# Kernel tuning notes

Measured on AMD Instinct MI355X. Metric: run time of the kernel, lower is better.

The kernel has to match this reference:

```python
import jax, jax.numpy as jnp
import numpy as np

N = 65536      # nodes (256x256 grid)
E = 1048576    # edges (avg degree 16)
T_IN = 10      # TIME_STEPS_IN
L = 64         # LATENT_DIMS
MID = 128      # LATENT_DIMS * MLP_RATIO
GD = 2         # grid dims


def _lin_init(key, fan_in, fan_out):
    kw, kb = jax.random.split(key)
    s = 1.0 / np.sqrt(fan_in)
    W = jax.random.uniform(kw, (fan_in, fan_out), jnp.float32, -s, s)
    b = jax.random.uniform(kb, (fan_out,), jnp.float32, -s, s)
    return W, b


def setup_inputs() -> dict:
    key = jax.random.key(0)
    ks = jax.random.split(key, 10)
    x = jax.random.normal(ks[0], (N, T_IN), jnp.float32)
    grid = jax.random.uniform(ks[1], (N, GD), jnp.float32)
    edge_index = jax.random.randint(ks[2], (2, E), 0, N, jnp.int64)
    W_proj1, b_proj1 = _lin_init(ks[3], T_IN + GD, MID)
    W_proj2, b_proj2 = _lin_init(ks[4], MID, L)
    Wk, bk = _lin_init(ks[5], 2 * L + 2 * GD + 1, L)   # K edge MLP (single linear)
    Ww, bw = _lin_init(ks[6], L, L)                     # W node MLP (single linear)
    W_dec1, b_dec1 = _lin_init(ks[7], L, MID)
    W_dec2, b_dec2 = _lin_init(ks[8], MID, 1)
    return {"x": x, "grid": grid, "edge_index": edge_index,
            "W_proj1": W_proj1, "b_proj1": b_proj1, "W_proj2": W_proj2, "b_proj2": b_proj2,
            "Wk": Wk, "bk": bk, "Ww": Ww, "bw": bw,
            "W_dec1": W_dec1, "b_dec1": b_dec1, "W_dec2": W_dec2, "b_dec2": b_dec2}


def _gelu(x):
    return jax.nn.gelu(x, approximate=False)  # torch F.gelu default = exact erf


def reference(x, grid, edge_index, W_proj1, b_proj1, W_proj2, b_proj2,
              Wk, bk, Ww, bw, W_dec1, b_dec1, W_dec2, b_dec2):
    # project: cat(x, grid) -> Linear -> GELU -> Linear
    h = jnp.concatenate([x, grid], axis=-1)               # [N, T_IN+2]
    h = _gelu(h @ W_proj1 + b_proj1) @ W_proj2 + b_proj2  # [N, L]

    # message passing block (PyG source_to_target: j = row 0, i = row 1)
    src = edge_index[0]
    dst = edge_index[1]
    x_j = h[src]                                          # [E, L]
    x_i = h[dst]                                          # [E, L]
    g_j = grid[src]                                       # [E, 2]
    g_i = grid[dst]                                       # [E, 2]
    dist = jnp.sqrt(jnp.sum(jnp.square(g_i - g_j), axis=-1, keepdims=True))  # [E, 1]
    ef = jnp.concatenate([dist, g_i, g_j, x_i, x_j], axis=-1)  # [E, 2L+5]
    msg = ef @ Wk + bk                                    # [E, L]
    aggr = jax.ops.segment_sum(msg, dst, num_segments=N)  # [N, L]
    h = _gelu(h @ Ww + bw + aggr)                         # update

    # decode: Linear -> GELU -> Linear
    out = _gelu(h @ W_dec1 + b_dec1) @ W_dec2 + b_dec2    # [N, 1]
    return out
```

## Files before the change

kernel.cpp:

```cpp
#include <hip/hip_runtime.h>
#include <hip/hip_fp16.h>

static __device__ __forceinline__ float gelu(float x) {
    return 0.5f * x * (1.0f + erff(x * 0.70710678118654752f));
}

#define CAPR 32

typedef _Float16 v8h __attribute__((ext_vector_type(8)));
typedef float    v4f __attribute__((ext_vector_type(4)));
typedef int      v4i __attribute__((ext_vector_type(4)));
union F8 { uint4 u; v8h v; _Float16 f[8]; };

static __device__ __forceinline__ void acc8(float* a, uint4 u) {
    float2 f0 = __half22float2(*(__half2*)&u.x);
    float2 f1 = __half22float2(*(__half2*)&u.y);
    float2 f2 = __half22float2(*(__half2*)&u.z);
    float2 f3 = __half22float2(*(__half2*)&u.w);
    a[0] += f0.x; a[1] += f0.y; a[2] += f1.x; a[3] += f1.y;
    a[4] += f2.x; a[5] += f2.y; a[6] += f3.x; a[7] += f3.y;
}

static __device__ __forceinline__ uint4 pack8(const float* v) {
    __half2 p0 = __floats2half2_rn(v[0], v[1]);
    __half2 p1 = __floats2half2_rn(v[2], v[3]);
    __half2 p2 = __floats2half2_rn(v[4], v[5]);
    __half2 p3 = __floats2half2_rn(v[6], v[7]);
    uint4 u;
    u.x = *(unsigned*)&p0; u.y = *(unsigned*)&p1;
    u.z = *(unsigned*)&p2; u.w = *(unsigned*)&p3;
    return u;
}

__global__ void __launch_bounds__(256, 4)
k_enc_scat(const float* __restrict__ x,
           const float* __restrict__ grid,
           const float* __restrict__ W1,
           const float* __restrict__ b1,
           const float* __restrict__ W2,
           const float* __restrict__ b2,
           const int* __restrict__ ei, int* __restrict__ cnt,
           unsigned short* __restrict__ ssrc,
           __half* __restrict__ h16, int N, int E, int scatB)
{
    __shared__ uint4 tabW2[1024];
    __shared__ __half wmids[4 * 16 * 136];
    int tid = threadIdx.x;

    if ((int)blockIdx.x < scatB) {
        int p = blockIdx.x & 7;
        int c = blockIdx.x >> 3;
        const v4i* s4 = (const v4i*)ei;
        const v4i* d4 = (const v4i*)(ei + E);
        int g4 = (E / (scatB >> 3)) >> 2;
        int base4 = c * g4;
        int shift = 31 - __clz(N >> 3);
#pragma unroll 8
        for (int g = 0; g < g4 / 256; g++) {
            int idx = base4 + g * 256 + tid;
            v4i d = __builtin_nontemporal_load(&d4[idx]);
            v4i s = __builtin_nontemporal_load(&s4[idx]);
            int q;
            if ((d[0] >> shift) == p) {
                q = atomicAdd(&cnt[(d[0] << 1) + 0], 1);
                if (q < CAPR) ssrc[((size_t)d[0] << 6) + q] = (unsigned short)s[0];
            }
            if ((d[1] >> shift) == p) {
                q = atomicAdd(&cnt[(d[1] << 1) + 1], 1);
                if (q < CAPR) ssrc[((size_t)d[1] << 6) + 32 + q] = (unsigned short)s[1];
            }
            if ((d[2] >> shift) == p) {
                q = atomicAdd(&cnt[(d[2] << 1) + 0], 1);
                if (q < CAPR) ssrc[((size_t)d[2] << 6) + q] = (unsigned short)s[2];
            }
            if ((d[3] >> shift) == p) {
                q = atomicAdd(&cnt[(d[3] << 1) + 1], 1);
                if (q < CAPR) ssrc[((size_t)d[3] << 6) + 32 + q] = (unsigned short)s[3];
            }
        }
        return;
    }

    int eb = blockIdx.x - scatB;
    int lane = tid & 63, wave = tid >> 6;
    int m = lane & 15, quad = lane >> 4;

    F8 w1f[8];
#pragma unroll
    for (int nt = 0; nt < 8; nt++) {
        int col = nt * 16 + m;
        int k0 = quad << 3;
#pragma unroll
        for (int j = 0; j < 8; j++)
            w1f[nt].f[j] = (k0 + j < 12) ? (_Float16)W1[(k0 + j) * 128 + col] : (_Float16)0.f;
    }

    for (int idx = tid; idx < 1024; idx += 256) {
        int l2 = idx & 63, nt = (idx >> 6) & 3, kc = idx >> 8;
        int col = nt * 16 + (l2 & 15);
        int k0 = kc * 32 + ((l2 >> 4) << 3);
        F8 f;
#pragma unroll
        for (int j = 0; j < 8; j++) f.f[j] = (_Float16)W2[(k0 + j) * 64 + col];
        tabW2[idx] = f.u;
    }
    __syncthreads();

    __half* wm = &wmids[wave * 16 * 136];

    for (int t = 0; t < 2; t++) {
        int tile = eb * 8 + wave * 2 + t;
        int base = tile * 16;
        int n = base + m;
        F8 a1;
#pragma unroll
        for (int j = 0; j < 8; j++) a1.f[j] = (_Float16)0.f;
        if (quad == 0) {
            float2 x0 = *(const float2*)&x[(size_t)n * 10 + 0];
            float2 x1 = *(const float2*)&x[(size_t)n * 10 + 2];
            float2 x2 = *(const float2*)&x[(size_t)n * 10 + 4];
            float2 x3 = *(const float2*)&x[(size_t)n * 10 + 6];
            a1.f[0] = (_Float16)x0.x; a1.f[1] = (_Float16)x0.y;
            a1.f[2] = (_Float16)x1.x; a1.f[3] = (_Float16)x1.y;
            a1.f[4] = (_Float16)x2.x; a1.f[5] = (_Float16)x2.y;
            a1.f[6] = (_Float16)x3.x; a1.f[7] = (_Float16)x3.y;
        } else if (quad == 1) {
            float2 x4 = *(const float2*)&x[(size_t)n * 10 + 8];
            float2 g  = *(const float2*)&grid[(size_t)n * 2];
            a1.f[0] = (_Float16)x4.x; a1.f[1] = (_Float16)x4.y;
            a1.f[2] = (_Float16)g.x;  a1.f[3] = (_Float16)g.y;
        }
#pragma unroll
        for (int nt = 0; nt < 8; nt++) {
            int col = nt * 16 + m;
            float b = b1[col];
            v4f acc = {b, b, b, b};
            acc = __builtin_amdgcn_mfma_f32_16x16x32_f16(a1.v, w1f[nt].v, acc, 0, 0, 0);
#pragma unroll
            for (int reg = 0; reg < 4; reg++)
                wm[(quad * 4 + reg) * 136 + col] = __float2half(gelu(acc[reg]));
        }
        __syncthreads();

        F8 a2[4];
#pragma unroll
        for (int kc = 0; kc < 4; kc++)
            a2[kc].u = *(const uint4*)&wm[m * 136 + kc * 32 + quad * 8];
#pragma unroll
        for (int nt = 0; nt < 4; nt++) {
            int col = nt * 16 + m;
            float b = b2[col];
            v4f acc = {b, b, b, b};
#pragma unroll
            for (int kc = 0; kc < 4; kc++) {
                F8 bf; bf.u = tabW2[kc * 256 + nt * 64 + lane];
                acc = __builtin_amdgcn_mfma_f32_16x16x32_f16(a2[kc].v, bf.v, acc, 0, 0, 0);
            }
#pragma unroll
            for (int reg = 0; reg < 4; reg++)
                h16[(size_t)(base + quad * 4 + reg) * 64 + col] = __float2half(acc[reg]);
        }
        __syncthreads();
    }
}

__global__ void k_gather(const __half* __restrict__ h16,
                         const float* __restrict__ grid,
                         const unsigned short* __restrict__ ssrc,
                         const int* __restrict__ cnt,
                         __half* __restrict__ sum_h16, float* __restrict__ sum_g,
                         float* __restrict__ sum_d, int N)
{
    int tid = blockIdx.x * blockDim.x + threadIdx.x;
    int n = tid >> 3;
    int l = tid & 7;
    if (n >= N) return;
    int2 cv = *(const int2*)&cnt[n << 1];
    const uint4* h8 = (const uint4*)h16;
    float a[8] = {0,0,0,0,0,0,0,0};
    float sgx = 0.f, sgy = 0.f, sd = 0.f;
    float gix = grid[2 * n], giy = grid[2 * n + 1];
#pragma unroll
    for (int r = 0; r < 2; r++) {
        int dg = min((r == 0) ? cv.x : cv.y, CAPR);
        const unsigned short* sr = ssrc + ((size_t)n << 6) + (r << 5);
        for (int i = 0; i < dg; i += 4) {
            ushort4 sv = *(const ushort4*)&sr[i];
            int sx = sv.x, sy = sv.y, sz = sv.z, sw = sv.w;
            int rem = dg - i;
            if (rem < 4) {
                if (rem <= 1) sy = sx;
                if (rem <= 2) sz = sx;
                sw = (rem <= 3) ? sx : sw;
            }
            uint4 u0 = h8[(size_t)sx * 8 + l];
            uint4 u1 = h8[(size_t)sy * 8 + l];
            uint4 u2 = h8[(size_t)sz * 8 + l];
            uint4 u3 = h8[(size_t)sw * 8 + l];
            acc8(a, u0);
            if (rem > 1) acc8(a, u1);
            if (rem > 2) acc8(a, u2);
            if (rem > 3) acc8(a, u3);
            if (l < 4 && i + l < dg) {
                int sj = (l == 0) ? sx : (l == 1) ? sy : (l == 2) ? sz : sw;
                float2 g = *(const float2*)&grid[2 * sj];
                float dx = gix - g.x, dy = giy - g.y;
                sd += sqrtf(dx * dx + dy * dy);
                sgx += g.x; sgy += g.y;
            }
        }
    }
    sd  += __shfl_xor(sd, 1);  sd  += __shfl_xor(sd, 2);  sd  += __shfl_xor(sd, 4);
    sgx += __shfl_xor(sgx, 1); sgx += __shfl_xor(sgx, 2); sgx += __shfl_xor(sgx, 4);
    sgy += __shfl_xor(sgy, 1); sgy += __shfl_xor(sgy, 2); sgy += __shfl_xor(sgy, 4);
    ((uint4*)(sum_h16 + (size_t)n * 64))[l] = pack8(a);
    if (l == 0) { sum_d[n] = sd; sum_g[2 * n] = sgx; sum_g[2 * n + 1] = sgy; }
}

__global__ void __launch_bounds__(256, 1)
k_updec(const __half* __restrict__ h16, const __half* __restrict__ sum_h16,
        const float* __restrict__ sum_g, const float* __restrict__ sum_d,
        const int* __restrict__ cnt, const float* __restrict__ grid,
        const float* __restrict__ Wk, const float* __restrict__ bk,
        const float* __restrict__ Ww, const float* __restrict__ bw,
        const float* __restrict__ Wd1, const float* __restrict__ bd1,
        const float* __restrict__ Wd2, const float* __restrict__ bd2,
        float* __restrict__ out, int N)
{
    __shared__ uint4 tabW[512];
    __shared__ uint4 tabC[512];
    __shared__ uint4 tabD[512];
    __shared__ uint4 tabV[256];
    __shared__ uint4 tabE[1024];
    __shared__ __half h2t[4 * 16 * 72];
    int tid = threadIdx.x;

    for (int idx = tid; idx < 512; idx += 256) {
        int lane = idx & 63, nt = (idx >> 6) & 3, kc = idx >> 8;
        int col = nt * 16 + (lane & 15);
        int kr  = kc * 32 + ((lane >> 4) << 3);
        F8 fw, fc, fd;
#pragma unroll
        for (int j = 0; j < 8; j++) {
            fw.f[j] = (_Float16)Ww[(kr + j) * 64 + col];
            fc.f[j] = (_Float16)Wk[(size_t)(5 + kr + j) * 64 + col];
            fd.f[j] = (_Float16)Wk[(size_t)(69 + kr + j) * 64 + col];
        }
        tabW[idx] = fw.u; tabC[idx] = fc.u; tabD[idx] = fd.u;
    }
    if (tid < 256) {
        int lane = tid & 63, nt = tid >> 6;
        int col = nt * 16 + (lane & 15);
        F8 fv;
#pragma unroll
        for (int j = 0; j < 8; j++) fv.f[j] = (_Float16)0.f;
        if ((lane >> 4) == 0) {
            fv.f[0] = (_Float16)bw[col];
            fv.f[1] = (_Float16)bk[col];
            fv.f[2] = (_Float16)Wk[col];
            fv.f[3] = (_Float16)Wk[64 + col];
            fv.f[4] = (_Float16)Wk[128 + col];
            fv.f[5] = (_Float16)Wk[192 + col];
            fv.f[6] = (_Float16)Wk[256 + col];
        }
        tabV[tid] = fv.u;
    }
    for (int idx = tid; idx < 1024; idx += 256) {
        int lane = idx & 63, nt = (idx >> 6) & 7, kc = idx >> 9;
        int col = nt * 16 + (lane & 15);
        int kr  = kc * 32 + ((lane >> 4) << 3);
        F8 f;
#pragma unroll
        for (int j = 0; j < 8; j++) f.f[j] = (_Float16)Wd1[(kr + j) * 128 + col];
        tabE[idx] = f.u;
    }
    __syncthreads();

    int lane = tid & 63, wave = tid >> 6;
    int m = lane & 15, quad = lane >> 4;
    const uint4* h8 = (const uint4*)h16;
    const uint4* s8 = (const uint4*)sum_h16;
    __half* wt = &h2t[wave * 16 * 72];
    float bd2v = bd2[0];

    for (int t = 0; t < 2; t++) {
        int tile = blockIdx.x * 8 + wave * 2 + t;
        int base = tile * 16;
        int n = base + m;
        int2 cv = *(const int2*)&cnt[n << 1];
        float deg = (float)(min(cv.x, CAPR) + min(cv.y, CAPR));
        float sd  = sum_d[n];
        float sgx = sum_g[2 * n], sgy = sum_g[2 * n + 1];
        float gix = grid[2 * n] * deg, giy = grid[2 * n + 1] * deg;

        F8 ah0, ah1, as0, as1, ahd0, ahd1, au;
        ah0.u = h8[(size_t)n * 8 + quad];
        ah1.u = h8[(size_t)n * 8 + 4 + quad];
        as0.u = s8[(size_t)n * 8 + quad];
        as1.u = s8[(size_t)n * 8 + 4 + quad];
        _Float16 dh = (_Float16)deg;
#pragma unroll
        for (int j = 0; j < 8; j++) { ahd0.f[j] = ah0.f[j] * dh; ahd1.f[j] = ah1.f[j] * dh; }
        float z = (quad == 0) ? 1.f : 0.f;
        au.f[0] = (_Float16)z;          au.f[1] = (_Float16)(deg * z);
        au.f[2] = (_Float16)(sd * z);   au.f[3] = (_Float16)(gix * z);
        au.f[4] = (_Float16)(giy * z);  au.f[5] = (_Float16)(sgx * z);
        au.f[6] = (_Float16)(sgy * z);  au.f[7] = (_Float16)0.f;

#pragma unroll
        for (int nt = 0; nt < 4; nt++) {
            F8 bv, bw0, bw1, bc0, bc1, bd0, bd1f;
            bv.u  = tabV[nt * 64 + lane];
            bw0.u = tabW[nt * 64 + lane];       bw1.u = tabW[256 + nt * 64 + lane];
            bc0.u = tabC[nt * 64 + lane];       bc1.u = tabC[256 + nt * 64 + lane];
            bd0.u = tabD[nt * 64 + lane];       bd1f.u = tabD[256 + nt * 64 + lane];
            v4f acc = {0.f, 0.f, 0.f, 0.f};
            acc = __builtin_amdgcn_mfma_f32_16x16x32_f16(au.v,   bv.v,   acc, 0, 0, 0);
            acc = __builtin_amdgcn_mfma_f32_16x16x32_f16(ah0.v,  bw0.v,  acc, 0, 0, 0);
            acc = __builtin_amdgcn_mfma_f32_16x16x32_f16(ah1.v,  bw1.v,  acc, 0, 0, 0);
            acc = __builtin_amdgcn_mfma_f32_16x16x32_f16(ahd0.v, bc0.v,  acc, 0, 0, 0);
            acc = __builtin_amdgcn_mfma_f32_16x16x32_f16(ahd1.v, bc1.v,  acc, 0, 0, 0);
            acc = __builtin_amdgcn_mfma_f32_16x16x32_f16(as0.v,  bd0.v,  acc, 0, 0, 0);
            acc = __builtin_amdgcn_mfma_f32_16x16x32_f16(as1.v,  bd1f.v, acc, 0, 0, 0);
#pragma unroll
            for (int reg = 0; reg < 4; reg++)
                wt[(quad * 4 + reg) * 72 + m + 16 * nt] = __float2half(gelu(acc[reg]));
        }
        __syncthreads();

        F8 dh0, dh1;
        dh0.u = *(const uint4*)&wt[m * 72 + quad * 8];
        dh1.u = *(const uint4*)&wt[m * 72 + 32 + quad * 8];
        float p[4] = {0.f, 0.f, 0.f, 0.f};
#pragma unroll
        for (int nt = 0; nt < 8; nt++) {
            int col = m + 16 * nt;
            float b = bd1[col];
            float w2 = Wd2[col];
            F8 b0, b1;
            b0.u = tabE[nt * 64 + lane];
            b1.u = tabE[512 + nt * 64 + lane];
            v4f acc = {b, b, b, b};
            acc = __builtin_amdgcn_mfma_f32_16x16x32_f16(dh0.v, b0.v, acc, 0, 0, 0);
            acc = __builtin_amdgcn_mfma_f32_16x16x32_f16(dh1.v, b1.v, acc, 0, 0, 0);
#pragma unroll
            for (int reg = 0; reg < 4; reg++) p[reg] += gelu(acc[reg]) * w2;
        }
#pragma unroll
        for (int reg = 0; reg < 4; reg++) {
            p[reg] += __shfl_xor(p[reg], 1);
            p[reg] += __shfl_xor(p[reg], 2);
            p[reg] += __shfl_xor(p[reg], 4);
            p[reg] += __shfl_xor(p[reg], 8);
        }
        if (m == 0) {
#pragma unroll
            for (int reg = 0; reg < 4; reg++)
                out[base + quad * 4 + reg] = p[reg] + bd2v;
        }
        __syncthreads();
    }
}

extern "C" void kernel_launch(void* const* d_in, const int* in_sizes, int n_in,
                              void* d_out, int out_size, void* d_ws, size_t ws_size,
                              hipStream_t stream)
{
    const float* x    = (const float*)d_in[0];
    const float* grid = (const float*)d_in[1];
    const int*   ei   = (const int*)d_in[2];
    const float* W1   = (const float*)d_in[3];
    const float* b1   = (const float*)d_in[4];
    const float* W2   = (const float*)d_in[5];
    const float* b2   = (const float*)d_in[6];
    const float* Wk   = (const float*)d_in[7];
    const float* bk   = (const float*)d_in[8];
    const float* Ww   = (const float*)d_in[9];
    const float* bw   = (const float*)d_in[10];
    const float* Wd1  = (const float*)d_in[11];
    const float* bd1  = (const float*)d_in[12];
    const float* Wd2  = (const float*)d_in[13];
    const float* bd2  = (const float*)d_in[14];
    float* out = (float*)d_out;

    int N = in_sizes[0] / 10;
    int E = in_sizes[2] / 2;

    char* ws = (char*)d_ws;
    size_t o_h16  = 0;
    size_t o_sh16 = o_h16  + (size_t)N * 64 * 2;
    size_t o_sumg = o_sh16 + (size_t)N * 64 * 2;
    size_t o_sumd = o_sumg + (size_t)N * 2 * 4;
    size_t o_cnt  = o_sumd + (size_t)N * 4;
    size_t o_ssrc = o_cnt  + (size_t)N * 2 * 4;

    __half* h16     = (__half*)(ws + o_h16);
    __half* sum_h16 = (__half*)(ws + o_sh16);
    float* sum_g = (float*)(ws + o_sumg);
    float* sum_d = (float*)(ws + o_sumd);
    int*   cnt   = (int*)  (ws + o_cnt);
    unsigned short* ssrc = (unsigned short*)(ws + o_ssrc);

    hipMemsetAsync(cnt, 0, (size_t)N * 2 * 4, stream);

    int scatB = E / (256 * 4);
    int encB  = (N / 16) / 8;
    k_enc_scat<<<dim3(scatB + encB), dim3(256), 0, stream>>>(x, grid, W1, b1, W2, b2,
                                                             ei, cnt, ssrc, h16, N, E, scatB);
    k_gather<<<dim3((N * 8 + 255) / 256), dim3(256), 0, stream>>>(h16, grid, ssrc, cnt,
                                                                   sum_h16, sum_g, sum_d, N);
    int tiles = N / 16;
    k_updec<<<dim3(tiles / 8), dim3(256), 0, stream>>>(h16, sum_h16, sum_g, sum_d, cnt,
                                                       grid, Wk, bk, Ww, bw,
                                                       Wd1, bd1, Wd2, bd2, out, N);
}
```

Baseline: 206.1 us.

## Fuse neighbor gather into update/decode kernel, dropping intermediate sum buffers

Merges the gather kernel into the update/decode kernel so each wave accumulates neighbor features for its 16-node tile in registers, then feeds them straight into the MFMA update and decoder. This removes the sum_h16/sum_g/sum_d round trip through global memory and one kernel launch. The trade-off is lower gather parallelism: each lane now handles two uint4 chunks per neighbor, with 4 lanes per node instead of 8. Each block also has to rebuild the shared-memory weight tables, and twice as many blocks are launched (one tile per wave). The bias/small-weight table moves from shared memory into registers.

```diff
diff --git a/kernel.cpp b/kernel.cpp
--- a/kernel.cpp
+++ b/kernel.cpp
@@ -164,22 +164,78 @@
     }
 }
 
-__global__ void k_gather(const __half* __restrict__ h16,
-                         const float* __restrict__ grid,
-                         const unsigned short* __restrict__ ssrc,
-                         const int* __restrict__ cnt,
-                         __half* __restrict__ sum_h16, float* __restrict__ sum_g,
-                         float* __restrict__ sum_d, int N)
+__global__ void __launch_bounds__(256, 1)
+k_gupdec(const __half* __restrict__ h16,
+         const unsigned short* __restrict__ ssrc,
+         const int* __restrict__ cnt, const float* __restrict__ grid,
+         const float* __restrict__ Wk, const float* __restrict__ bk,
+         const float* __restrict__ Ww, const float* __restrict__ bw,
+         const float* __restrict__ Wd1, const float* __restrict__ bd1,
+         const float* __restrict__ Wd2, const float* __restrict__ bd2,
+         float* __restrict__ out, int N)
 {
-    int tid = blockIdx.x * blockDim.x + threadIdx.x;
-    int n = tid >> 3;
-    int l = tid & 7;
-    if (n >= N) return;
+    __shared__ uint4 tabW[512];
+    __shared__ uint4 tabC[512];
+    __shared__ uint4 tabD[512];
+    __shared__ uint4 tabE[1024];
+    __shared__ __half h2t[4 * 16 * 72];
+    int tid = threadIdx.x;
+    int lane = tid & 63, wave = tid >> 6;
+    int m = lane & 15, quad = lane >> 4;
+
+    for (int idx = tid; idx < 512; idx += 256) {
+        int l2 = idx & 63, nt = (idx >> 6) & 3, kc = idx >> 8;
+        int col = nt * 16 + (l2 & 15);
+        int kr  = kc * 32 + ((l2 >> 4) << 3);
+        F8 fw, fc, fd;
+#pragma unroll
+        for (int j = 0; j < 8; j++) {
+            fw.f[j] = (_Float16)Ww[(kr + j) * 64 + col];
+            fc.f[j] = (_Float16)Wk[(size_t)(5 + kr + j) * 64 + col];
+            fd.f[j] = (_Float16)Wk[(size_t)(69 + kr + j) * 64 + col];
+        }
+        tabW[idx] = fw.u; tabC[idx] = fc.u; tabD[idx] = fd.u;
+    }
+    for (int idx = tid; idx < 1024; idx += 256) {
+        int l2 = idx & 63, nt = (idx >> 6) & 7, kc = idx >> 9;
+        int col = nt * 16 + (l2 & 15);
+        int kr  = kc * 32 + ((l2 >> 4) << 3);
+        F8 f;
+#pragma unroll
+        for (int j = 0; j < 8; j++) f.f[j] = (_Float16)Wd1[(kr + j) * 128 + col];
+        tabE[idx] = f.u;
+    }
+    F8 vreg[4];
+#pragma unroll
+    for (int nt = 0; nt < 4; nt++) {
+        int col = nt * 16 + m;
+#pragma unroll
+        for (int j = 0; j < 8; j++) vreg[nt].f[j] = (_Float16)0.f;
+        if (quad == 0) {
+            vreg[nt].f[0] = (_Float16)bw[col];
+            vreg[nt].f[1] = (_Float16)bk[col];
+            vreg[nt].f[2] = (_Float16)Wk[col];
+            vreg[nt].f[3] = (_Float16)Wk[64 + col];
+            vreg[nt].f[4] = (_Float16)Wk[128 + col];
+            vreg[nt].f[5] = (_Float16)Wk[192 + col];
+            vreg[nt].f[6] = (_Float16)Wk[256 + col];
+        }
+    }
+    __syncthreads();
+
+    const uint4* h8 = (const uint4*)h16;
+    __half* wt = &h2t[wave * 16 * 72];
+    float bd2v = bd2[0];
+
+    int tile = blockIdx.x * 4 + wave;
+    int base = tile * 16;
+    int n = base + m;
     int2 cv = *(const int2*)&cnt[n << 1];
-    const uint4* h8 = (const uint4*)h16;
-    float a[8] = {0,0,0,0,0,0,0,0};
+    float gix0 = grid[2 * n], giy0 = grid[2 * n + 1];
+
+    float a0[8] = {0,0,0,0,0,0,0,0};
+    float a1g[8] = {0,0,0,0,0,0,0,0};
     float sgx = 0.f, sgy = 0.f, sd = 0.f;
-    float gix = grid[2 * n], giy = grid[2 * n + 1];
 #pragma unroll
     for (int r = 0; r < 2; r++) {
         int dg = min((r == 0) ? cv.x : cv.y, CAPR);
@@ -193,172 +249,100 @@
                 if (rem <= 2) sz = sx;
                 sw = (rem <= 3) ? sx : sw;
             }
-            uint4 u0 = h8[(size_t)sx * 8 + l];
-            uint4 u1 = h8[(size_t)sy * 8 + l];
-            uint4 u2 = h8[(size_t)sz * 8 + l];
-            uint4 u3 = h8[(size_t)sw * 8 + l];
-            acc8(a, u0);
-            if (rem > 1) acc8(a, u1);
-            if (rem > 2) acc8(a, u2);
-            if (rem > 3) acc8(a, u3);
-            if (l < 4 && i + l < dg) {
-                int sj = (l == 0) ? sx : (l == 1) ? sy : (l == 2) ? sz : sw;
+            uint4 u;
+            u = h8[(size_t)sx * 8 + quad];     acc8(a0, u);
+            u = h8[(size_t)sx * 8 + 4 + quad]; acc8(a1g, u);
+            if (rem > 1) {
+                u = h8[(size_t)sy * 8 + quad];     acc8(a0, u);
+                u = h8[(size_t)sy * 8 + 4 + quad]; acc8(a1g, u);
+            }
+            if (rem > 2) {
+                u = h8[(size_t)sz * 8 + quad];     acc8(a0, u);
+                u = h8[(size_t)sz * 8 + 4 + quad]; acc8(a1g, u);
+            }
+            if (rem > 3) {
+                u = h8[(size_t)sw * 8 + quad];     acc8(a0, u);
+                u = h8[(size_t)sw * 8 + 4 + quad]; acc8(a1g, u);
+            }
+            if (i + quad < dg) {
+                int sj = (quad == 0) ? sx : (quad == 1) ? sy : (quad == 2) ? sz : sw;
                 float2 g = *(const float2*)&grid[2 * sj];
-                float dx = gix - g.x, dy = giy - g.y;
+                float dx = gix0 - g.x, dy = giy0 - g.y;
                 sd += sqrtf(dx * dx + dy * dy);
                 sgx += g.x; sgy += g.y;
             }
         }
     }
-    sd  += __shfl_xor(sd, 1);  sd  += __shfl_xor(sd, 2);  sd  += __shfl_xor(sd, 4);
-    sgx += __shfl_xor(sgx, 1); sgx += __shfl_xor(sgx, 2); sgx += __shfl_xor(sgx, 4);
-    sgy += __shfl_xor(sgy, 1); sgy += __shfl_xor(sgy, 2); sgy += __shfl_xor(sgy, 4);
-    ((uint4*)(sum_h16 + (size_t)n * 64))[l] = pack8(a);
-    if (l == 0) { sum_d[n] = sd; sum_g[2 * n] = sgx; sum_g[2 * n + 1] = sgy; }
-}
-
-__global__ void __launch_bounds__(256, 1)
-k_updec(const __half* __restrict__ h16, const __half* __restrict__ sum_h16,
-        const float* __restrict__ sum_g, const float* __restrict__ sum_d,
-        const int* __restrict__ cnt, const float* __restrict__ grid,
-        const float* __restrict__ Wk, const float* __restrict__ bk,
-        const float* __restrict__ Ww, const float* __restrict__ bw,
-        const float* __restrict__ Wd1, const float* __restrict__ bd1,
-        const float* __restrict__ Wd2, const float* __restrict__ bd2,
-        float* __restrict__ out, int N)
-{
-    __shared__ uint4 tabW[512];
-    __shared__ uint4 tabC[512];
-    __shared__ uint4 tabD[512];
-    __shared__ uint4 tabV[256];
-    __shared__ uint4 tabE[1024];
-    __shared__ __half h2t[4 * 16 * 72];
-    int tid = threadIdx.x;
-
-    for (int idx = tid; idx < 512; idx += 256) {
-        int lane = idx & 63, nt = (idx >> 6) & 3, kc = idx >> 8;
-        int col = nt * 16 + (lane & 15);
-        int kr  = kc * 32 + ((lane >> 4) << 3);
-        F8 fw, fc, fd;
-#pragma unroll
-        for (int j = 0; j < 8; j++) {
-            fw.f[j] = (_Float16)Ww[(kr + j) * 64 + col];
-            fc.f[j] = (_Float16)Wk[(size_t)(5 + kr + j) * 64 + col];
-            fd.f[j] = (_Float16)Wk[(size_t)(69 + kr + j) * 64 + col];
-        }
-        tabW[idx] = fw.u; tabC[idx] = fc.u; tabD[idx] = fd.u;
-    }
-    if (tid < 256) {
-        int lane = tid & 63, nt = tid >> 6;
-        int col = nt * 16 + (lane & 15);
-        F8 fv;
-#pragma unroll
-        for (int j = 0; j < 8; j++) fv.f[j] = (_Float16)0.f;
-        if ((lane >> 4) == 0) {
-            fv.f[0] = (_Float16)bw[col];
-            fv.f[1] = (_Float16)bk[col];
-            fv.f[2] = (_Float16)Wk[col];
-            fv.f[3] = (_Float16)Wk[64 + col];
-            fv.f[4] = (_Float16)Wk[128 + col];
-            fv.f[5] = (_Float16)Wk[192 + col];
-            fv.f[6] = (_Float16)Wk[256 + col];
-        }
-        tabV[tid] = fv.u;
-    }
-    for (int idx = tid; idx < 1024; idx += 256) {
-        int lane = idx & 63, nt = (idx >> 6) & 7, kc = idx >> 9;
-        int col = nt * 16 + (lane & 15);
-        int kr  = kc * 32 + ((lane >> 4) << 3);
-        F8 f;
-#pragma unroll
-        for (int j = 0; j < 8; j++) f.f[j] = (_Float16)Wd1[(kr + j) * 128 + col];
-        tabE[idx] = f.u;
+    sd  += __shfl_xor(sd, 16);  sd  += __shfl_xor(sd, 32);
+    sgx += __shfl_xor(sgx, 16); sgx += __shfl_xor(sgx, 32);
+    sgy += __shfl_xor(sgy, 16); sgy += __shfl_xor(sgy, 32);
+
+    float deg = (float)(min(cv.x, CAPR) + min(cv.y, CAPR));
+    float gix = gix0 * deg, giy = giy0 * deg;
+
+    F8 ah0, ah1, as0, as1, ahd0, ahd1, au;
+    ah0.u = h8[(size_t)n * 8 + quad];
+    ah1.u = h8[(size_t)n * 8 + 4 + quad];
+    as0.u = pack8(a0);
+    as1.u = pack8(a1g);
+    _Float16 dh = (_Float16)deg;
+#pragma unroll
+    for (int j = 0; j < 8; j++) { ahd0.f[j] = ah0.f[j] * dh; ahd1.f[j] = ah1.f[j] * dh; }
+    float z = (quad == 0) ? 1.f : 0.f;
+    au.f[0] = (_Float16)z;          au.f[1] = (_Float16)(deg * z);
+    au.f[2] = (_Float16)(sd * z);   au.f[3] = (_Float16)(gix * z);
+    au.f[4] = (_Float16)(giy * z);  au.f[5] = (_Float16)(sgx * z);
+    au.f[6] = (_Float16)(sgy * z);  au.f[7] = (_Float16)0.f;
+
+#pragma unroll
+    for (int nt = 0; nt < 4; nt++) {
+        F8 bw0, bw1, bc0, bc1, bd0, bd1f;
+        bw0.u = tabW[nt * 64 + lane];       bw1.u = tabW[256 + nt * 64 + lane];
+        bc0.u = tabC[nt * 64 + lane];       bc1.u = tabC[256 + nt * 64 + lane];
+        bd0.u = tabD[nt * 64 + lane];       bd1f.u = tabD[256 + nt * 64 + lane];
+        v4f acc = {0.f, 0.f, 0.f, 0.f};
+        acc = __builtin_amdgcn_mfma_f32_16x16x32_f16(au.v,   vreg[nt].v, acc, 0, 0, 0);
+        acc = __builtin_amdgcn_mfma_f32_16x16x32_f16(ah0.v,  bw0.v,  acc, 0, 0, 0);
+        acc = __builtin_amdgcn_mfma_f32_16x16x32_f16(ah1.v,  bw1.v,  acc, 0, 0, 0);
+        acc = __builtin_amdgcn_mfma_f32_16x16x32_f16(ahd0.v, bc0.v,  acc, 0, 0, 0);
+        acc = __builtin_amdgcn_mfma_f32_16x16x32_f16(ahd1.v, bc1.v,  acc, 0, 0, 0);
+        acc = __builtin_amdgcn_mfma_f32_16x16x32_f16(as0.v,  bd0.v,  acc, 0, 0, 0);
+        acc = __builtin_amdgcn_mfma_f32_16x16x32_f16(as1.v,  bd1f.v, acc, 0, 0, 0);
+#pragma unroll
+        for (int reg = 0; reg < 4; reg++)
+            wt[(quad * 4 + reg) * 72 + m + 16 * nt] = __float2half(gelu(acc[reg]));
     }
     __syncthreads();
 
-    int lane = tid & 63, wave = tid >> 6;
-    int m = lane & 15, quad = lane >> 4;
-    const uint4* h8 = (const uint4*)h16;
-    const uint4* s8 = (const uint4*)sum_h16;
-    __half* wt = &h2t[wave * 16 * 72];
-    float bd2v = bd2[0];
-
-    for (int t = 0; t < 2; t++) {
-        int tile = blockIdx.x * 8 + wave * 2 + t;
-        int base = tile * 16;
-        int n = base + m;
-        int2 cv = *(const int2*)&cnt[n << 1];
-        float deg = (float)(min(cv.x, CAPR) + min(cv.y, CAPR));
-        float sd  = sum_d[n];
-        float sgx = sum_g[2 * n], sgy = sum_g[2 * n + 1];
-        float gix = grid[2 * n] * deg, giy = grid[2 * n + 1] * deg;
-
-        F8 ah0, ah1, as0, as1, ahd0, ahd1, au;
-        ah0.u = h8[(size_t)n * 8 + quad];
-        ah1.u = h8[(size_t)n * 8 + 4 + quad];
-        as0.u = s8[(size_t)n * 8 + quad];
-        as1.u = s8[(size_t)n * 8 + 4 + quad];
-        _Float16 dh = (_Float16)deg;
-#pragma unroll
-        for (int j = 0; j < 8; j++) { ahd0.f[j] = ah0.f[j] * dh; ahd1.f[j] = ah1.f[j] * dh; }
-        float z = (quad == 0) ? 1.f : 0.f;
-        au.f[0] = (_Float16)z;          au.f[1] = (_Float16)(deg * z);
-        au.f[2] = (_Float16)(sd * z);   au.f[3] = (_Float16)(gix * z);
-        au.f[4] = (_Float16)(giy * z);  au.f[5] = (_Float16)(sgx * z);
-        au.f[6] = (_Float16)(sgy * z);  au.f[7] = (_Float16)0.f;
-
-#pragma unroll
-        for (int nt = 0; nt < 4; nt++) {
-            F8 bv, bw0, bw1, bc0, bc1, bd0, bd1f;
-            bv.u  = tabV[nt * 64 + lane];
-            bw0.u = tabW[nt * 64 + lane];       bw1.u = tabW[256 + nt * 64 + lane];
-            bc0.u = tabC[nt * 64 + lane];       bc1.u = tabC[256 + nt * 64 + lane];
-            bd0.u = tabD[nt * 64 + lane];       bd1f.u = tabD[256 + nt * 64 + lane];
-            v4f acc = {0.f, 0.f, 0.f, 0.f};
-            acc = __builtin_amdgcn_mfma_f32_16x16x32_f16(au.v,   bv.v,   acc, 0, 0, 0);
-            acc = __builtin_amdgcn_mfma_f32_16x16x32_f16(ah0.v,  bw0.v,  acc, 0, 0, 0);
-            acc = __builtin_amdgcn_mfma_f32_16x16x32_f16(ah1.v,  bw1.v,  acc, 0, 0, 0);
-            acc = __builtin_amdgcn_mfma_f32_16x16x32_f16(ahd0.v, bc0.v,  acc, 0, 0, 0);
-            acc = __builtin_amdgcn_mfma_f32_16x16x32_f16(ahd1.v, bc1.v,  acc, 0, 0, 0);
-            acc = __builtin_amdgcn_mfma_f32_16x16x32_f16(as0.v,  bd0.v,  acc, 0, 0, 0);
-            acc = __builtin_amdgcn_mfma_f32_16x16x32_f16(as1.v,  bd1f.v, acc, 0, 0, 0);
-#pragma unroll
-            for (int reg = 0; reg < 4; reg++)
-                wt[(quad * 4 + reg) * 72 + m + 16 * nt] = __float2half(gelu(acc[reg]));
-        }
-        __syncthreads();
-
-        F8 dh0, dh1;
-        dh0.u = *(const uint4*)&wt[m * 72 + quad * 8];
-        dh1.u = *(const uint4*)&wt[m * 72 + 32 + quad * 8];
-        float p[4] = {0.f, 0.f, 0.f, 0.f};
-#pragma unroll
-        for (int nt = 0; nt < 8; nt++) {
-            int col = m + 16 * nt;
-            float b = bd1[col];
-            float w2 = Wd2[col];
-            F8 b0, b1;
-            b0.u = tabE[nt * 64 + lane];
-            b1.u = tabE[512 + nt * 64 + lane];
-            v4f acc = {b, b, b, b};
-            acc = __builtin_amdgcn_mfma_f32_16x16x32_f16(dh0.v, b0.v, acc, 0, 0, 0);
-            acc = __builtin_amdgcn_mfma_f32_16x16x32_f16(dh1.v, b1.v, acc, 0, 0, 0);
-#pragma unroll
-            for (int reg = 0; reg < 4; reg++) p[reg] += gelu(acc[reg]) * w2;
-        }
-#pragma unroll
-        for (int reg = 0; reg < 4; reg++) {
-            p[reg] += __shfl_xor(p[reg], 1);
-            p[reg] += __shfl_xor(p[reg], 2);
-            p[reg] += __shfl_xor(p[reg], 4);
-            p[reg] += __shfl_xor(p[reg], 8);
-        }
-        if (m == 0) {
-#pragma unroll
-            for (int reg = 0; reg < 4; reg++)
-                out[base + quad * 4 + reg] = p[reg] + bd2v;
-        }
-        __syncthreads();
+    F8 dh0, dh1;
+    dh0.u = *(const uint4*)&wt[m * 72 + quad * 8];
+    dh1.u = *(const uint4*)&wt[m * 72 + 32 + quad * 8];
+    float p[4] = {0.f, 0.f, 0.f, 0.f};
+#pragma unroll
+    for (int nt = 0; nt < 8; nt++) {
+        int col = m + 16 * nt;
+        float b = bd1[col];
+        float w2 = Wd2[col];
+        F8 b0, b1;
+        b0.u = tabE[nt * 64 + lane];
+        b1.u = tabE[512 + nt * 64 + lane];
+        v4f acc = {b, b, b, b};
+        acc = __builtin_amdgcn_mfma_f32_16x16x32_f16(dh0.v, b0.v, acc, 0, 0, 0);
+        acc = __builtin_amdgcn_mfma_f32_16x16x32_f16(dh1.v, b1.v, acc, 0, 0, 0);
+#pragma unroll
+        for (int reg = 0; reg < 4; reg++) p[reg] += gelu(acc[reg]) * w2;
+    }
+#pragma unroll
+    for (int reg = 0; reg < 4; reg++) {
+        p[reg] += __shfl_xor(p[reg], 1);
+        p[reg] += __shfl_xor(p[reg], 2);
+        p[reg] += __shfl_xor(p[reg], 4);
+        p[reg] += __shfl_xor(p[reg], 8);
+    }
+    if (m == 0) {
+#pragma unroll
+        for (int reg = 0; reg < 4; reg++)
+            out[base + quad * 4 + reg] = p[reg] + bd2v;
     }
 }
 
@@ -388,17 +372,11 @@
 
     char* ws = (char*)d_ws;
     size_t o_h16  = 0;
-    size_t o_sh16 = o_h16  + (size_t)N * 64 * 2;
-    size_t o_sumg = o_sh16 + (size_t)N * 64 * 2;
-    size_t o_sumd = o_sumg + (size_t)N * 2 * 4;
-    size_t o_cnt  = o_sumd + (size_t)N * 4;
-    size_t o_ssrc = o_cnt  + (size_t)N * 2 * 4;
-
-    __half* h16     = (__half*)(ws + o_h16);
-    __half* sum_h16 = (__half*)(ws + o_sh16);
-    float* sum_g = (float*)(ws + o_sumg);
-    float* sum_d = (float*)(ws + o_sumd);
-    int*   cnt   = (int*)  (ws + o_cnt);
+    size_t o_cnt  = o_h16 + (size_t)N * 64 * 2;
+    size_t o_ssrc = o_cnt + (size_t)N * 2 * 4;
+
+    __half* h16 = (__half*)(ws + o_h16);
+    int*    cnt = (int*)  (ws + o_cnt);
     unsigned short* ssrc = (unsigned short*)(ws + o_ssrc);
 
     hipMemsetAsync(cnt, 0, (size_t)N * 2 * 4, stream);
@@ -407,10 +385,8 @@
     int encB  = (N / 16) / 8;
     k_enc_scat<<<dim3(scatB + encB), dim3(256), 0, stream>>>(x, grid, W1, b1, W2, b2,
                                                              ei, cnt, ssrc, h16, N, E, scatB);
-    k_gather<<<dim3((N * 8 + 255) / 256), dim3(256), 0, stream>>>(h16, grid, ssrc, cnt,
-                                                                   sum_h16, sum_g, sum_d, N);
     int tiles = N / 16;
-    k_updec<<<dim3(tiles / 8), dim3(256), 0, stream>>>(h16, sum_h16, sum_g, sum_d, cnt,
-                                                       grid, Wk, bk, Ww, bw,
-                                                       Wd1, bd1, Wd2, bd2, out, N);
-}
+    k_gupdec<<<dim3(tiles / 4), dim3(256), 0, stream>>>(h16, ssrc, cnt, grid,
+                                                        Wk, bk, Ww, bw,
+                                                        Wd1, bd1, Wd2, bd2, out, N);
+}
```

Result: slower. 224.8 us (+9.1%).
